# Optimization experiments

Measured on AMD Instinct MI355X. Metric: run time of the kernel, lower is better.

Reference implementation:

```python
import jax, jax.numpy as jnp
import numpy as np

P = 8  # patch size
EPS = 1e-5

def ln_ch(x, w, b):
    # WithBias LayerNorm over channel dim of (B,C,H,W): torch code flattens to (B,HW,C) and norms last dim
    mu = x.mean(axis=1, keepdims=True)
    var = ((x - mu) ** 2).mean(axis=1, keepdims=True)
    return (x - mu) / jnp.sqrt(var + EPS) * w[None, :, None, None] + b[None, :, None, None]

def conv1x1(x, w):
    # w: [C_out, C_in]
    return jnp.einsum('bchw,oc->bohw', x, w)

def dwconv3x3(x, w):
    # depthwise 3x3, w: [C,1,3,3]
    return jax.lax.conv_general_dilated(x, w, (1, 1), 'SAME', dimension_numbers=('NCHW', 'OIHW', 'NCHW'), feature_group_count=x.shape[1])

def patchify(x):
    b, c, H, W = x.shape
    return x.reshape(b, c, H // P, P, W // P, P).transpose(0, 1, 2, 4, 3, 5)  # b c h w p1 p2

def unpatchify(x):
    b, c, h, w, p1, p2 = x.shape
    return x.transpose(0, 1, 2, 4, 3, 5).reshape(b, c, h * p1, w * p2)

def setup_inputs() -> dict:
    key = jax.random.key(0)
    ks = jax.random.split(key, 16)
    B, C, H, W = 4, 64, 256, 256
    hid = 2 * C  # ffn_expansion_factor=2
    s = 0.02
    return {
        'x': jax.random.normal(ks[0], (B, C, H, W), jnp.float32),
        'evt': jax.random.normal(ks[1], (B, C, H, W), jnp.float32),
        'ln1i_w': jnp.ones((C,), jnp.float32), 'ln1i_b': jnp.zeros((C,), jnp.float32),
        'ln1e_w': jnp.ones((C,), jnp.float32), 'ln1e_b': jnp.zeros((C,), jnp.float32),
        'w_q': jax.random.normal(ks[2], (2 * C, C), jnp.float32) * s,
        'dw_q': jax.random.normal(ks[3], (2 * C, 1, 3, 3), jnp.float32) * s,
        'w_kv': jax.random.normal(ks[4], (4 * C, C), jnp.float32) * s,
        'dw_kv': jax.random.normal(ks[5], (4 * C, 1, 3, 3), jnp.float32) * s,
        'lnA_w': jnp.ones((2 * C,), jnp.float32), 'lnA_b': jnp.zeros((2 * C,), jnp.float32),
        'w_po_attn': jax.random.normal(ks[6], (C, 2 * C), jnp.float32) * s,
        'ln2_w': jnp.ones((C,), jnp.float32), 'ln2_b': jnp.zeros((C,), jnp.float32),
        'w_pi': jax.random.normal(ks[7], (2 * hid, C), jnp.float32) * s,
        'fft_param': jnp.ones((2 * hid, 1, 1, P, P // 2 + 1), jnp.float32),
        'dw_ffn': jax.random.normal(ks[8], (2 * hid, 1, 3, 3), jnp.float32) * s,
        'w_po_ffn': jax.random.normal(ks[9], (C, hid), jnp.float32) * s,
    }

def reference(x, evt, ln1i_w, ln1i_b, ln1e_w, ln1e_b, w_q, dw_q, w_kv, dw_kv, lnA_w, lnA_b, w_po_attn, ln2_w, ln2_b, w_pi, fft_param, dw_ffn, w_po_ffn):
    # ---- EventFSAS cross attention ----
    xn = ln_ch(x, ln1i_w, ln1i_b)
    en = ln_ch(evt, ln1e_w, ln1e_b)
    q = dwconv3x3(conv1x1(xn, w_q), dw_q)               # (B,2C,H,W)
    kv = dwconv3x3(conv1x1(en, w_kv), dw_kv)            # (B,4C,H,W)
    k, v = jnp.split(kv, 2, axis=1)
    qf = jnp.fft.rfft2(patchify(q))                      # (B,2C,h,w,8,5) complex
    kf = jnp.fft.rfft2(patchify(k))
    out = jnp.fft.irfft2(qf * kf, s=(P, P))
    out = ln_ch(unpatchify(out), lnA_w, lnA_b)
    x = x + conv1x1(v * out, w_po_attn)
    # ---- DFFN ----
    y = conv1x1(ln_ch(x, ln2_w, ln2_b), w_pi)            # (B,4C,H,W)
    yf = jnp.fft.rfft2(patchify(y)) * fft_param
    y = unpatchify(jnp.fft.irfft2(yf, s=(P, P)))
    y = dwconv3x3(y, dw_ffn)
    y1, y2 = jnp.split(y, 2, axis=1)
    y = jax.nn.gelu(y1, approximate=False) * y2          # torch nn.GELU is exact erf form
    return x + conv1x1(y, w_po_ffn)
```

## Files before the change

kernel.cpp:

```cpp
#include <hip/hip_runtime.h>

#define HW 65536
#define NPOS 262144

typedef unsigned int   u32;
typedef unsigned short u16;
typedef __attribute__((ext_vector_type(8))) short v8s;
typedef __attribute__((ext_vector_type(4))) float f32x4;
typedef __attribute__((ext_vector_type(2))) float f32x2;

__device__ __forceinline__ float bf2f(u16 h){
  union { u32 u; float f; } c; c.u = ((u32)h) << 16; return c.f;
}
__device__ __forceinline__ u16 f2bf(float f){
  union { u32 u; float f; } c; c.f = f;
  u32 r = c.u + 0x7fffu + ((c.u >> 16) & 1u);
  return (u16)(r >> 16);
}
__device__ __forceinline__ u32 pk2(float a, float b){
  return (u32)f2bf(a) | ((u32)f2bf(b) << 16);
}
__device__ __forceinline__ v8s as8(uint4 u){
  union { uint4 a; v8s b; } c; c.a = u; return c.b;
}
__device__ __forceinline__ f32x2 up2(u32 u){
  union { u32 u; float f; } lo, hi;
  lo.u = u << 16; hi.u = u & 0xffff0000u;
  f32x2 r; r.x = lo.f; r.y = hi.f; return r;
}
__device__ __forceinline__ float gelu_exact(float x){
  return 0.5f*x*(1.0f+erff(x*0.70710678118654752f));
}

__device__ void fold_w(const float* __restrict__ W, int rows,
                       const float* __restrict__ lw, const float* __restrict__ lb,
                       u16* __restrict__ Wf, float* __restrict__ A, float* __restrict__ B){
  int tid = threadIdx.x;
  for (int e = tid; e < rows*64; e += 256) Wf[e] = f2bf(lw[e & 63] * W[e]);
  for (int r = tid; r < rows; r += 256){
    float a = 0.f, b2 = 0.f;
    for (int c = 0; c < 64; c++){ float w = W[r*64+c]; a += lw[c]*w; b2 += lb[c]*w; }
    A[r] = a; B[r] = b2;
  }
}

__global__ void k_prep(const float* __restrict__ M, float* __restrict__ g,
    const float* wq,  const float* l1iw, const float* l1ib, u16* wqf,  float* aq,  float* bq,
    const float* wkv, const float* l1ew, const float* l1eb, u16* wkvf, float* akv, float* bkv,
    const float* wpi, const float* l2w,  const float* l2b,  u16* wpif, float* api, float* bpi,
    const float* wpa, u16* wpaf, const float* wpf, u16* wpff)
{
  int blk = blockIdx.x, tid = threadIdx.x;
  if (blk < 64){
    int t = blk*256 + tid;
    int c = t >> 6, uv = t & 63, u = uv >> 3, v = uv & 7;
    const float* mc = M + c*40;
    const float ctab[8] = {1.f, 0.70710678118654752f, 0.f, -0.70710678118654752f,
                           -1.f, -0.70710678118654752f, 0.f, 0.70710678118654752f};
    float acc = 0.f;
    for (int k1=0;k1<8;k1++)
      for (int k2=0;k2<8;k2++){
        float s = (k2<=4) ? mc[k1*5+k2] : mc[(((8-k1)&7)*5) + (8-k2)];
        acc += s * ctab[(k1*u + k2*v)&7];
      }
    g[t] = acc * (1.f/64.f);
  } else if (blk == 64){ fold_w(wq, 128, l1iw, l1ib, wqf, aq, bq); }
  else if (blk == 65){ fold_w(wkv, 256, l1ew, l1eb, wkvf, akv, bkv); }
  else if (blk == 66){ fold_w(wpi, 256, l2w, l2b, wpif, api, bpi); }
  else if (blk == 67){ for (int e=tid; e<64*128; e+=256) wpaf[e] = f2bf(wpa[e]); }
  else               { for (int e=tid; e<64*128; e+=256) wpff[e] = f2bf(wpf[e]); }
}

__global__ void k_prep2(const float* __restrict__ g, u16* __restrict__ CM){
  int c = blockIdx.x;
  const float* gc = g + (size_t)c*64;
  u16* cm = CM + (size_t)c*4096;
  for (int e = threadIdx.x; e < 4096; e += 256){
    int o = e >> 6, i = e & 63;
    int du = ((o>>3) - (i>>3)) & 7, dv = ((o&7) - (i&7)) & 7;
    cm[e] = f2bf(gc[du*8 + dv]);
  }
}

struct GA {
  const float* src; const u16* Wf; const float* Af; const float* Bf;
  u32* dst; int o0; int dstOffP; int Cdp; int b0; int pxbase;
};

template<int NZ>
__global__ __launch_bounds__(256) void k_gemm64(GA a0, GA a1){
  GA a = (blockIdx.y == 0) ? a0 : a1;
  __shared__ uint4 lsX[128*8];
  __shared__ uint4 lsW[64*NZ*8];
  __shared__ float2 sPart[256];
  __shared__ float2 sStat[128];
  int tid = threadIdx.x;
  int px = tid & 127, hf = tid >> 7;
  int p0 = a.pxbase + blockIdx.x*128;
  int b = p0 >> 16, hwb = p0 & 65535;
  {
    const uint4* wsrc = (const uint4*)(a.Wf + (size_t)a.o0*64);
    #pragma unroll
    for (int i=0; i<NZ*2; i++){
      int idx = i*256 + tid, row = idx>>3, s = idx&7;
      lsW[row*8 + (s ^ (row&7))] = wsrc[idx];
    }
  }
  {
    const float* sp = a.src + (size_t)b*64*HW + hwb + px + (size_t)(hf*32)*HW;
    float e[32];
    #pragma unroll
    for (int c=0;c<32;c++) e[c] = sp[(size_t)c*HW];
    float sm = 0.f, sq = 0.f;
    #pragma unroll
    for (int c=0;c<32;c++){ sm += e[c]; sq += e[c]*e[c]; }
    uint4* xrow = lsX + px*8;
    #pragma unroll
    for (int sl=0; sl<4; sl++){
      uint4 pkv;
      pkv.x = pk2(e[sl*8+0], e[sl*8+1]); pkv.y = pk2(e[sl*8+2], e[sl*8+3]);
      pkv.z = pk2(e[sl*8+4], e[sl*8+5]); pkv.w = pk2(e[sl*8+6], e[sl*8+7]);
      xrow[(hf*4+sl) ^ (px&7)] = pkv;
    }
    sPart[tid] = make_float2(sm, sq);
  }
  __syncthreads();
  if (tid < 128){
    float2 A = sPart[tid], B = sPart[tid+128];
    float s = A.x + B.x, q = A.y + B.y;
    float mu = s*(1.f/64.f);
    float var = q*(1.f/64.f) - mu*mu;
    sStat[tid] = make_float2(mu, rsqrtf(fmaxf(var,0.f)+1e-5f));
  }
  __syncthreads();
  int w = tid>>6, l = tid&63, g = l>>4, c15 = l&15;
  float2 stv[2];
  #pragma unroll
  for (int pp=0;pp<2;pp++) stv[pp] = sStat[w*32 + pp*16 + c15];

  #pragma unroll
  for (int z=0; z<NZ; z++){
    f32x4 acc[2][4];
    #pragma unroll
    for (int pp=0;pp<2;pp++)
      #pragma unroll
      for (int po=0;po<4;po++) acc[pp][po] = (f32x4){0.f,0.f,0.f,0.f};
    #pragma unroll
    for (int kk=0; kk<2; kk++){
      v8s wf[4], xf[2];
      #pragma unroll
      for (int po=0;po<4;po++){ int row = z*64 + po*16 + c15; wf[po] = as8(lsW[row*8 + ((kk*4+g) ^ (row&7))]); }
      #pragma unroll
      for (int pp=0;pp<2;pp++){ int row = w*32 + pp*16 + c15; xf[pp] = as8(lsX[row*8 + ((kk*4+g) ^ (row&7))]); }
      #pragma unroll
      for (int pp=0;pp<2;pp++)
        #pragma unroll
        for (int po=0;po<4;po++)
          acc[pp][po] = __builtin_amdgcn_mfma_f32_16x16x32_bf16(wf[po], xf[pp], acc[pp][po], 0,0,0);
    }
    size_t obaseP = ((size_t)(b - a.b0)*a.Cdp + a.dstOffP + z*32)*HW + hwb + w*32;
    #pragma unroll
    for (int po=0;po<4;po++)
      #pragma unroll
      for (int j2=0;j2<2;j2++){
        int oc = po*16 + g*4 + j2*2;
        float A0 = a.Af[a.o0 + z*64 + oc],   B0 = a.Bf[a.o0 + z*64 + oc];
        float A1 = a.Af[a.o0 + z*64 + oc+1], B1 = a.Bf[a.o0 + z*64 + oc+1];
        int ocp = po*8 + g*2 + j2;
        u32* dp = a.dst + obaseP + (size_t)ocp*HW + c15;
        #pragma unroll
        for (int pp=0;pp<2;pp++){
          float lo = stv[pp].y*(acc[pp][po][j2*2  ] - stv[pp].x*A0) + B0;
          float hi = stv[pp].y*(acc[pp][po][j2*2+1] - stv[pp].x*A1) + B1;
          dp[pp*16] = pk2(lo, hi);
        }
      }
  }
}

__global__ __launch_bounds__(256) void k_gemm_attn(
    const float* __restrict__ x, const u32* __restrict__ orawp, const u32* __restrict__ vbp,
    const float* __restrict__ lnw, const float* __restrict__ lnb,
    const u16* __restrict__ Wf, float* __restrict__ out)
{
  __shared__ uint4 lsX[128*16];
  __shared__ uint4 lsW[64*16];
  __shared__ float2 sPart[256];
  __shared__ float2 sStat[128];
  int tid = threadIdx.x;
  int p0 = blockIdx.x*128;
  int b = p0 >> 16, hwb = p0 & 65535;
  int px = tid & 127, hf = tid >> 7;
  {
    const uint4* wsrc = (const uint4*)Wf;
    #pragma unroll
    for (int i=0;i<4;i++){
      int idx = i*256 + tid, row = idx>>4, s = idx&15;
      lsW[row*16 + (s ^ (row&15))] = wsrc[idx];
    }
  }
  const u32* orp = orawp + ((size_t)b*64 + hf*32)*HW + hwb + px;
  {
    u32 r32[32];
    #pragma unroll
    for (int i=0;i<32;i++) r32[i] = orp[(size_t)i*HW];
    float sum = 0.f, ssq = 0.f;
    #pragma unroll
    for (int sl=0; sl<8; sl++){
      u32 wds[4];
      #pragma unroll
      for (int q2=0;q2<4;q2++){
        u32 wv = r32[sl*4+q2];
        float fl = bf2f((u16)(wv&0xffff)), fh = bf2f((u16)(wv>>16));
        sum += fl + fh; ssq += fl*fl + fh*fh;
        wds[q2] = wv;
      }
      int s = hf*8 + sl;
      lsX[px*16 + (s ^ (px&15))] = make_uint4(wds[0],wds[1],wds[2],wds[3]);
    }
    sPart[tid] = make_float2(sum, ssq);
  }
  __syncthreads();
  if (tid < 128){
    float2 A = sPart[tid], B = sPart[tid+128];
    float s = A.x + B.x, q = A.y + B.y;
    float mu = s*(1.f/128.f);
    float var = q*(1.f/128.f) - mu*mu;
    sStat[tid] = make_float2(mu, rsqrtf(fmaxf(var,0.f)+1e-5f));
  }
  __syncthreads();
  {
    float2 st = sStat[px];
    const u32* vp = vbp + ((size_t)b*64 + hf*32)*HW + hwb + px;
    u32 v32[32];
    #pragma unroll
    for (int i=0;i<32;i++) v32[i] = vp[(size_t)i*HW];
    #pragma unroll
    for (int sl=0; sl<8; sl++){
      int s = hf*8 + sl;
      int li = px*16 + (s ^ (px&15));
      uint4 raw = lsX[li];
      u32 wds[4] = {raw.x, raw.y, raw.z, raw.w};
      u32 ow[4];
      #pragma unroll
      for (int q2=0;q2<4;q2++){
        int ch = hf*64 + sl*8 + q2*2;
        float e0 = bf2f((u16)(wds[q2]&0xffff)), e1 = bf2f((u16)(wds[q2]>>16));
        u32 vv = v32[sl*4+q2];
        float v0 = bf2f((u16)(vv&0xffff)), v1 = bf2f((u16)(vv>>16));
        float r0 = ((e0-st.x)*st.y*lnw[ch  ] + lnb[ch  ])*v0;
        float r1 = ((e1-st.x)*st.y*lnw[ch+1] + lnb[ch+1])*v1;
        ow[q2] = pk2(r0, r1);
      }
      lsX[li] = make_uint4(ow[0],ow[1],ow[2],ow[3]);
    }
  }
  __syncthreads();
  int w4 = tid>>6, l = tid&63, g = l>>4, c15 = l&15;
  f32x4 acc[2][4];
  #pragma unroll
  for (int pp=0;pp<2;pp++)
    #pragma unroll
    for (int po=0;po<4;po++) acc[pp][po] = (f32x4){0.f,0.f,0.f,0.f};
  #pragma unroll
  for (int kk=0; kk<4; kk++){
    v8s wf[4], xf[2];
    #pragma unroll
    for (int po=0;po<4;po++){ int row = po*16 + c15; wf[po] = as8(lsW[row*16 + ((kk*4+g) ^ (row&15))]); }
    #pragma unroll
    for (int pp=0;pp<2;pp++){ int row = w4*32 + pp*16 + c15; xf[pp] = as8(lsX[row*16 + ((kk*4+g) ^ (row&15))]); }
    #pragma unroll
    for (int pp=0;pp<2;pp++)
      #pragma unroll
      for (int po=0;po<4;po++)
        acc[pp][po] = __builtin_amdgcn_mfma_f32_16x16x32_bf16(wf[po], xf[pp], acc[pp][po], 0,0,0);
  }
  size_t obase = (size_t)b*64*HW + hwb + w4*32;
  #pragma unroll
  for (int po=0;po<4;po++)
    #pragma unroll
    for (int j=0;j<4;j++){
      int oc = po*16 + g*4 + j;
      const float* xs = x + obase + (size_t)oc*HW + c15;
      float* dp = out + obase + (size_t)oc*HW + c15;
      #pragma unroll
      for (int pp=0;pp<2;pp++) dp[pp*16] = xs[pp*16] + acc[pp][po][j];
    }
}

__global__ __launch_bounds__(256) void k_gemm_ffn(
    const u32* __restrict__ y3gp, const u16* __restrict__ Wf, float* __restrict__ out,
    int pxbase, int b0)
{
  __shared__ uint4 lsX[128*16];
  __shared__ uint4 lsW[64*16];
  int tid = threadIdx.x;
  int p0 = pxbase + blockIdx.x*128;
  int b = p0 >> 16, hwb = p0 & 65535;
  int px = tid & 127, hf = tid >> 7;
  {
    const uint4* wsrc = (const uint4*)Wf;
    #pragma unroll
    for (int i=0;i<4;i++){
      int idx = i*256 + tid, row = idx>>4, s = idx&15;
      lsW[row*16 + (s ^ (row&15))] = wsrc[idx];
    }
  }
  const u32* yp = y3gp + ((size_t)(b-b0)*64 + hf*32)*HW + hwb + px;
  {
    u32 r32[32];
    #pragma unroll
    for (int i=0;i<32;i++) r32[i] = yp[(size_t)i*HW];
    #pragma unroll
    for (int sl=0; sl<8; sl++){
      int s = hf*8 + sl;
      lsX[px*16 + (s ^ (px&15))] = make_uint4(r32[sl*4+0],r32[sl*4+1],r32[sl*4+2],r32[sl*4+3]);
    }
  }
  __syncthreads();
  int w4 = tid>>6, l = tid&63, g = l>>4, c15 = l&15;
  f32x4 acc[2][4];
  #pragma unroll
  for (int pp=0;pp<2;pp++)
    #pragma unroll
    for (int po=0;po<4;po++) acc[pp][po] = (f32x4){0.f,0.f,0.f,0.f};
  #pragma unroll
  for (int kk=0; kk<4; kk++){
    v8s wf[4], xf[2];
    #pragma unroll
    for (int po=0;po<4;po++){ int row = po*16 + c15; wf[po] = as8(lsW[row*16 + ((kk*4+g) ^ (row&15))]); }
    #pragma unroll
    for (int pp=0;pp<2;pp++){ int row = w4*32 + pp*16 + c15; xf[pp] = as8(lsX[row*16 + ((kk*4+g) ^ (row&15))]); }
    #pragma unroll
    for (int pp=0;pp<2;pp++)
      #pragma unroll
      for (int po=0;po<4;po++)
        acc[pp][po] = __builtin_amdgcn_mfma_f32_16x16x32_bf16(wf[po], xf[pp], acc[pp][po], 0,0,0);
  }
  size_t obase = (size_t)b*64*HW + hwb + w4*32;
  #pragma unroll
  for (int po=0;po<4;po++)
    #pragma unroll
    for (int j=0;j<4;j++){
      int oc = po*16 + g*4 + j;
      float* dp = out + obase + (size_t)oc*HW + c15;
      #pragma unroll
      for (int pp=0;pp<2;pp++) dp[pp*16] = dp[pp*16] + acc[pp][po][j];
    }
}

__device__ __forceinline__ void dw8p_acc2(const u32* __restrict__ sp,
    const float* __restrict__ w9lo, const float* __restrict__ w9hi,
    int h, int w8, f32x2 a2[8])
{
  #pragma unroll
  for (int r=0;r<3;r++){
    int hh = h + r - 1;
    if (hh < 0 || hh > 255) continue;
    const u32* rp = sp + hh*256 + w8;
    uint4 ua = *(const uint4*)rp;
    uint4 ub = *(const uint4*)(rp+4);
    u32 e[8] = {ua.x,ua.y,ua.z,ua.w,ub.x,ub.y,ub.z,ub.w};
    u32 lef = (w8 > 0)   ? rp[-1] : 0u;
    u32 rig = (w8 < 248) ? rp[8]  : 0u;
    f32x2 vm[10];
    vm[0] = up2(lef);
    #pragma unroll
    for (int j=0;j<8;j++) vm[j+1] = up2(e[j]);
    vm[9] = up2(rig);
    f32x2 wa = {w9lo[r*3  ], w9hi[r*3  ]};
    f32x2 wb = {w9lo[r*3+1], w9hi[r*3+1]};
    f32x2 wc = {w9lo[r*3+2], w9hi[r*3+2]};
    #pragma unroll
    for (int j=0;j<8;j++)
      a2[j] += vm[j]*wa + vm[j+1]*wb + vm[j+2]*wc;
  }
}

__global__ __launch_bounds__(256) void k_dw8p(
    const u32* __restrict__ src, const float* __restrict__ wgt, int c0,
    u32* __restrict__ dstp, int dstOffP)
{
  int t = blockIdx.x*256 + threadIdx.x;
  int w8 = (t & 31)*8, h = (t>>5) & 255;
  int plane = t >> 13;
  int pr = plane & 31, b = plane >> 5;
  const u32* sp = src + (size_t)plane*HW;
  const float* w9 = wgt + (size_t)(c0 + 2*pr)*9;
  f32x2 a2[8];
  #pragma unroll
  for (int j=0;j<8;j++) a2[j] = (f32x2){0.f,0.f};
  dw8p_acc2(sp, w9, w9+9, h, w8, a2);
  u32* dp = dstp + ((size_t)(b*64 + dstOffP + pr))*HW + h*256 + w8;
  uint4 s0, s1;
  s0.x=pk2(a2[0].x,a2[0].y); s0.y=pk2(a2[1].x,a2[1].y); s0.z=pk2(a2[2].x,a2[2].y); s0.w=pk2(a2[3].x,a2[3].y);
  s1.x=pk2(a2[4].x,a2[4].y); s1.y=pk2(a2[5].x,a2[5].y); s1.z=pk2(a2[6].x,a2[6].y); s1.w=pk2(a2[7].x,a2[7].y);
  *(uint4*)dp = s0; *(uint4*)(dp+4) = s1;
}

__global__ __launch_bounds__(256) void k_dw8gp(
    const u32* __restrict__ Y0p, const float* __restrict__ wgt, u32* __restrict__ Y3gp)
{
  int t = blockIdx.x*256 + threadIdx.x;
  int w8 = (t & 31)*8, h = (t>>5) & 255;
  int pc = t >> 13;
  int pr = pc & 63, bl = pc >> 6;
  const u32* spA = Y0p + ((size_t)(bl*128 + pr))*HW;
  const u32* spG = Y0p + ((size_t)(bl*128 + 64 + pr))*HW;
  const float* w9a = wgt + (size_t)(2*pr)*9;
  const float* w9g = wgt + (size_t)(128 + 2*pr)*9;
  f32x2 aA[8], aG[8];
  #pragma unroll
  for (int j=0;j<8;j++){ aA[j] = (f32x2){0.f,0.f}; aG[j] = (f32x2){0.f,0.f}; }
  dw8p_acc2(spA, w9a, w9a+9, h, w8, aA);
  dw8p_acc2(spG, w9g, w9g+9, h, w8, aG);
  u32* dp = Y3gp + ((size_t)(bl*64 + pr))*HW + h*256 + w8;
  uint4 s0, s1;
  s0.x=pk2(gelu_exact(aA[0].x)*aG[0].x, gelu_exact(aA[0].y)*aG[0].y);
  s0.y=pk2(gelu_exact(aA[1].x)*aG[1].x, gelu_exact(aA[1].y)*aG[1].y);
  s0.z=pk2(gelu_exact(aA[2].x)*aG[2].x, gelu_exact(aA[2].y)*aG[2].y);
  s0.w=pk2(gelu_exact(aA[3].x)*aG[3].x, gelu_exact(aA[3].y)*aG[3].y);
  s1.x=pk2(gelu_exact(aA[4].x)*aG[4].x, gelu_exact(aA[4].y)*aG[4].y);
  s1.y=pk2(gelu_exact(aA[5].x)*aG[5].x, gelu_exact(aA[5].y)*aG[5].y);
  s1.z=pk2(gelu_exact(aA[6].x)*aG[6].x, gelu_exact(aA[6].y)*aG[6].y);
  s1.w=pk2(gelu_exact(aA[7].x)*aG[7].x, gelu_exact(aA[7].y)*aG[7].y);
  *(uint4*)dp = s0; *(uint4*)(dp+4) = s1;
}

__global__ __launch_bounds__(256) void k_circqk4(
    const u32* __restrict__ bq, const u32* __restrict__ bk,
    const float* __restrict__ dwq, const float* __restrict__ dwk, int c0,
    u32* __restrict__ orawp, int oprBase)
{
  __shared__ f32x2 qd[8][288];
  __shared__ f32x2 kd[8][288];
  int tid = threadIdx.x;
  int p = tid & 31, i = tid >> 5;
  int pr = blockIdx.y, b = blockIdx.z;
  int h0 = blockIdx.x*8;
  const u32* qp = bq + ((size_t)(b*32+pr))*HW;
  const u32* kp = bk + ((size_t)(b*32+pr))*HW;
  const float* wq9 = dwq + (size_t)(c0 + 2*pr)*9;
  const float* wk9 = dwk + (size_t)(c0 + 2*pr)*9;
  {
    f32x2 a2[8];
    #pragma unroll
    for (int j=0;j<8;j++) a2[j] = (f32x2){0.f,0.f};
    dw8p_acc2(qp, wq9, wq9+9, h0+i, p*8, a2);
    #pragma unroll
    for (int j=0;j<8;j++) qd[i][p*9+j] = a2[j];
  }
  {
    f32x2 a2[8];
    #pragma unroll
    for (int j=0;j<8;j++) a2[j] = (f32x2){0.f,0.f};
    dw8p_acc2(kp, wk9, wk9+9, h0+i, p*8, a2);
    #pragma unroll
    for (int j=0;j<8;j++) kd[i][p*9+j] = a2[j];
  }
  __syncthreads();
  f32x2 o[8];
  #pragma unroll
  for (int j=0;j<8;j++) o[j] = (f32x2){0.f,0.f};
  #pragma unroll
  for (int u=0;u<8;u++){
    int ku = (i-u)&7;
    f32x2 qv[8], kr[8];
    #pragma unroll
    for (int v=0;v<8;v++) qv[v] = qd[u][p*9+v];
    #pragma unroll
    for (int e=0;e<8;e++) kr[e] = kd[ku][p*9+e];
    #pragma unroll
    for (int v=0;v<8;v++){
      f32x2 qq = qv[v];
      #pragma unroll
      for (int j=0;j<8;j++)
        o[j] += qq * kr[(j-v)&7];
    }
  }
  u32* op = orawp + ((size_t)(b*64 + oprBase + pr))*HW + (size_t)(h0+i)*256 + p*8;
  uint4 s0, s1;
  s0.x=pk2(o[0].x,o[0].y); s0.y=pk2(o[1].x,o[1].y); s0.z=pk2(o[2].x,o[2].y); s0.w=pk2(o[3].x,o[3].y);
  s1.x=pk2(o[4].x,o[4].y); s1.y=pk2(o[5].x,o[5].y); s1.z=pk2(o[6].x,o[6].y); s1.w=pk2(o[7].x,o[7].y);
  *(uint4*)op = s0; *(uint4*)(op+4) = s1;
}

__global__ __launch_bounds__(256) void k_circg_mfma(
    u32* __restrict__ y, const u16* __restrict__ CM)
{
  __shared__ uint4 lsA[2][64*8];
  __shared__ uint4 lsB[2][64*8];
  int tid = threadIdx.x;
  int pr = blockIdx.y, b = blockIdx.z;
  int h0 = blockIdx.x*16;
  u32* plane = y + ((size_t)(b*128+pr))*HW;
  {
    const uint4* cmsrc = (const uint4*)(CM + (size_t)(2*pr)*4096);
    #pragma unroll
    for (int t=0; t<4; t++){
      int idx = t*256 + tid;
      int ch = idx >> 9, e = idx & 511;
      int row = e >> 3, s = e & 7;
      lsA[ch][row*8 + (s ^ (row&7))] = cmsrc[ch*512 + e];
    }
  }
  {
    #pragma unroll
    for (int t=0; t<2; t++){
      int rr = t*256 + tid;
      int n = rr >> 3, i = rr & 7;
      const u32* rp = plane + (size_t)(h0 + (n>>5)*8 + i)*256 + (n&31)*8;
      uint4 ua = *(const uint4*)rp;
      uint4 ub = *(const uint4*)(rp+4);
      u32 e[8] = {ua.x,ua.y,ua.z,ua.w,ub.x,ub.y,ub.z,ub.w};
      uint4 L, H;
      L.x = (e[0]&0xffffu) | (e[1]<<16);
      L.y = (e[2]&0xffffu) | (e[3]<<16);
      L.z = (e[4]&0xffffu) | (e[5]<<16);
      L.w = (e[6]&0xffffu) | (e[7]<<16);
      H.x = (e[0]>>16) | (e[1]&0xffff0000u);
      H.y = (e[2]>>16) | (e[3]&0xffff0000u);
      H.z = (e[4]>>16) | (e[5]&0xffff0000u);
      H.w = (e[6]>>16) | (e[7]&0xffff0000u);
      lsB[0][n*8 + (i ^ (n&7))] = L;
      lsB[1][n*8 + (i ^ (n&7))] = H;
    }
  }
  __syncthreads();
  int w = tid>>6, l = tid&63, g = l>>4, c15 = l&15;
  f32x4 acc[2][4];
  #pragma unroll
  for (int ch=0;ch<2;ch++)
    #pragma unroll
    for (int po=0;po<4;po++) acc[ch][po] = (f32x4){0.f,0.f,0.f,0.f};
  #pragma unroll
  for (int kk=0; kk<2; kk++){
    v8s bfr[2];
    { int row = w*16 + c15;
      bfr[0] = as8(lsB[0][row*8 + ((kk*4+g) ^ (row&7))]);
      bfr[1] = as8(lsB[1][row*8 + ((kk*4+g) ^ (row&7))]); }
    #pragma unroll
    for (int po=0;po<4;po++){
      int row = po*16 + c15;
      v8s aL = as8(lsA[0][row*8 + ((kk*4+g) ^ (row&7))]);
      v8s aH = as8(lsA[1][row*8 + ((kk*4+g) ^ (row&7))]);
      acc[0][po] = __builtin_amdgcn_mfma_f32_16x16x32_bf16(aL, bfr[0], acc[0][po], 0,0,0);
      acc[1][po] = __builtin_amdgcn_mfma_f32_16x16x32_bf16(aH, bfr[1], acc[1][po], 0,0,0);
    }
  }
  int patch = w*16 + c15;
  u32* pbase = plane + (size_t)(h0 + (patch>>5)*8)*256 + (patch&31)*8;
  #pragma unroll
  for (int po=0;po<4;po++){
    int oh = po*2 + (g>>1), ow4 = 4*(g&1);
    uint4 sv;
    sv.x = pk2(acc[0][po][0], acc[1][po][0]);
    sv.y = pk2(acc[0][po][1], acc[1][po][1]);
    sv.z = pk2(acc[0][po][2], acc[1][po][2]);
    sv.w = pk2(acc[0][po][3], acc[1][po][3]);
    *(uint4*)(pbase + (size_t)oh*256 + ow4) = sv;
  }
}

extern "C" void kernel_launch(void* const* d_in, const int* in_sizes, int n_in,
                              void* d_out, int out_size, void* d_ws, size_t ws_size,
                              hipStream_t stream)
{
  const float* x       = (const float*)d_in[0];
  const float* evt     = (const float*)d_in[1];
  const float* ln1i_w  = (const float*)d_in[2];
  const float* ln1i_b  = (const float*)d_in[3];
  const float* ln1e_w  = (const float*)d_in[4];
  const float* ln1e_b  = (const float*)d_in[5];
  const float* w_q     = (const float*)d_in[6];
  const float* dw_q    = (const float*)d_in[7];
  const float* w_kv    = (const float*)d_in[8];
  const float* dw_kv   = (const float*)d_in[9];
  const float* lnA_w   = (const float*)d_in[10];
  const float* lnA_b   = (const float*)d_in[11];
  const float* w_po_at = (const float*)d_in[12];
  const float* ln2_w   = (const float*)d_in[13];
  const float* ln2_b   = (const float*)d_in[14];
  const float* w_pi    = (const float*)d_in[15];
  const float* fft_par = (const float*)d_in[16];
  const float* dw_ffn  = (const float*)d_in[17];
  const float* w_poffn = (const float*)d_in[18];
  float* out = (float*)d_out;

  char* ws = (char*)d_ws;
  const size_t MiB = 1048576ull;
  u32*   P1p   = (u32*)(ws);
  u32*   ORAWp = (u32*)(ws + 32*MiB);
  u32*   P2p   = (u32*)(ws + 96*MiB);
  u32*   VBUFp = (u32*)(ws + 96*MiB);
  u32*   Y0p   = (u32*)(ws);
  u32*   Y3Gp  = (u32*)(ws + 64*MiB);
  char* sm = ws + 160*MiB;
  float* G    = (float*)(sm);
  u16* WQF    = (u16*)(sm + 65536);
  u16* WKVF   = (u16*)(sm + 81920);
  u16* WPIF   = (u16*)(sm + 114688);
  u16* WPAF   = (u16*)(sm + 147456);
  u16* WPFF   = (u16*)(sm + 163840);
  float* AQ   = (float*)(sm + 180224);
  float* BQ   = (float*)(sm + 180736);
  float* AKV  = (float*)(sm + 181248);
  float* BKV  = (float*)(sm + 182272);
  float* API  = (float*)(sm + 183296);
  float* BPI  = (float*)(sm + 184320);
  u16* CMAT   = (u16*)(ws + 161*MiB);

  dim3 blk256(256);

  k_prep<<<69, blk256, 0, stream>>>(fft_par, G,
      w_q, ln1i_w, ln1i_b, WQF, AQ, BQ,
      w_kv, ln1e_w, ln1e_b, WKVF, AKV, BKV,
      w_pi, ln2_w, ln2_b, WPIF, API, BPI,
      w_po_at, WPAF, w_poffn, WPFF);
  k_prep2<<<256, blk256, 0, stream>>>(G, CMAT);

  for (int i=0;i<2;i++){
    GA qa = {x,   WQF,  AQ,  BQ,  P1p, 64*i, 0, 32, 0, 0};
    GA ka = {evt, WKVF, AKV, BKV, P2p, 64*i, 0, 32, 0, 0};
    k_gemm64<1><<<dim3(2048,2,1), blk256, 0, stream>>>(qa, ka);
    k_circqk4<<<dim3(32,32,4), blk256, 0, stream>>>(P1p, P2p, dw_q, dw_kv, 64*i, ORAWp, 32*i);
  }
  for (int i=0;i<2;i++){
    GA va = {evt, WKVF, AKV, BKV, P1p, 128+64*i, 0, 32, 0, 0};
    k_gemm64<1><<<dim3(2048,1,1), blk256, 0, stream>>>(va, va);
    k_dw8p<<<4096, blk256, 0, stream>>>(P1p, dw_kv, 128+64*i, VBUFp, 32*i);
  }
  k_gemm_attn<<<2048, blk256, 0, stream>>>(x, ORAWp, VBUFp, lnA_w, lnA_b, WPAF, out);

  for (int h=0;h<2;h++){
    GA pa = {out, WPIF, API, BPI, Y0p, 0, 0, 128, 2*h, h*131072};
    k_gemm64<4><<<dim3(1024,1,1), blk256, 0, stream>>>(pa, pa);
    k_circg_mfma<<<dim3(16,128,2), blk256, 0, stream>>>(Y0p, CMAT);
    k_dw8gp<<<4096, blk256, 0, stream>>>(Y0p, dw_ffn, Y3Gp);
    k_gemm_ffn<<<1024, blk256, 0, stream>>>(Y3Gp, WPFF, out, h*131072, 2*h);
  }
}
```

Baseline: 523.5 us.

## Process all Q/K/V channel chunks in one pass when workspace allows

When the workspace holds at least 200 MiB, the attention stage computes all 64 channel pairs per GEMM and circular-conv launch. This replaces the two half-width chunks, so it uses fewer launches and re-reads the x/evt inputs and layernorm stats fewer times. The workspace layout is remapped so the larger Q, K and ORAW buffers fit, and constant tables move to a higher offset. The old chunked path is kept as a fallback for smaller workspaces. Whether the new path runs depends on the workspace size the harness provides.

```diff
diff --git a/kernel.cpp b/kernel.cpp
--- a/kernel.cpp
+++ b/kernel.cpp
@@ -379,12 +379,12 @@
 
 __global__ __launch_bounds__(256) void k_dw8p(
     const u32* __restrict__ src, const float* __restrict__ wgt, int c0,
-    u32* __restrict__ dstp, int dstOffP)
+    u32* __restrict__ dstp, int dstOffP, int prMask, int prShift)
 {
   int t = blockIdx.x*256 + threadIdx.x;
   int w8 = (t & 31)*8, h = (t>>5) & 255;
   int plane = t >> 13;
-  int pr = plane & 31, b = plane >> 5;
+  int pr = plane & prMask, b = plane >> prShift;
   const u32* sp = src + (size_t)plane*HW;
   const float* w9 = wgt + (size_t)(c0 + 2*pr)*9;
   f32x2 a2[8];
@@ -430,7 +430,7 @@
 __global__ __launch_bounds__(256) void k_circqk4(
     const u32* __restrict__ bq, const u32* __restrict__ bk,
     const float* __restrict__ dwq, const float* __restrict__ dwk, int c0,
-    u32* __restrict__ orawp, int oprBase)
+    u32* __restrict__ orawp, int oprBase, int cpb)
 {
   __shared__ f32x2 qd[8][288];
   __shared__ f32x2 kd[8][288];
@@ -438,8 +438,8 @@
   int p = tid & 31, i = tid >> 5;
   int pr = blockIdx.y, b = blockIdx.z;
   int h0 = blockIdx.x*8;
-  const u32* qp = bq + ((size_t)(b*32+pr))*HW;
-  const u32* kp = bk + ((size_t)(b*32+pr))*HW;
+  const u32* qp = bq + ((size_t)(b*cpb+pr))*HW;
+  const u32* kp = bk + ((size_t)(b*cpb+pr))*HW;
   const float* wq9 = dwq + (size_t)(c0 + 2*pr)*9;
   const float* wk9 = dwk + (size_t)(c0 + 2*pr)*9;
   {
@@ -589,13 +589,9 @@
 
   char* ws = (char*)d_ws;
   const size_t MiB = 1048576ull;
-  u32*   P1p   = (u32*)(ws);
-  u32*   ORAWp = (u32*)(ws + 32*MiB);
-  u32*   P2p   = (u32*)(ws + 96*MiB);
-  u32*   VBUFp = (u32*)(ws + 96*MiB);
-  u32*   Y0p   = (u32*)(ws);
-  u32*   Y3Gp  = (u32*)(ws + 64*MiB);
-  char* sm = ws + 160*MiB;
+  bool big = (ws_size >= 200*MiB);
+  size_t smOff = big ? 192*MiB : 160*MiB;
+  char* sm = ws + smOff;
   float* G    = (float*)(sm);
   u16* WQF    = (u16*)(sm + 65536);
   u16* WKVF   = (u16*)(sm + 81920);
@@ -608,7 +604,7 @@
   float* BKV  = (float*)(sm + 182272);
   float* API  = (float*)(sm + 183296);
   float* BPI  = (float*)(sm + 184320);
-  u16* CMAT   = (u16*)(ws + 161*MiB);
+  u16* CMAT   = (u16*)(sm + 1*MiB);
 
   dim3 blk256(256);
 
@@ -619,24 +615,56 @@
       w_po_at, WPAF, w_poffn, WPFF);
   k_prep2<<<256, blk256, 0, stream>>>(G, CMAT);
 
-  for (int i=0;i<2;i++){
-    GA qa = {x,   WQF,  AQ,  BQ,  P1p, 64*i, 0, 32, 0, 0};
-    GA ka = {evt, WKVF, AKV, BKV, P2p, 64*i, 0, 32, 0, 0};
-    k_gemm64<1><<<dim3(2048,2,1), blk256, 0, stream>>>(qa, ka);
-    k_circqk4<<<dim3(32,32,4), blk256, 0, stream>>>(P1p, P2p, dw_q, dw_kv, 64*i, ORAWp, 32*i);
-  }
-  for (int i=0;i<2;i++){
-    GA va = {evt, WKVF, AKV, BKV, P1p, 128+64*i, 0, 32, 0, 0};
-    k_gemm64<1><<<dim3(2048,1,1), blk256, 0, stream>>>(va, va);
-    k_dw8p<<<4096, blk256, 0, stream>>>(P1p, dw_kv, 128+64*i, VBUFp, 32*i);
-  }
-  k_gemm_attn<<<2048, blk256, 0, stream>>>(x, ORAWp, VBUFp, lnA_w, lnA_b, WPAF, out);
-
-  for (int h=0;h<2;h++){
-    GA pa = {out, WPIF, API, BPI, Y0p, 0, 0, 128, 2*h, h*131072};
-    k_gemm64<4><<<dim3(1024,1,1), blk256, 0, stream>>>(pa, pa);
-    k_circg_mfma<<<dim3(16,128,2), blk256, 0, stream>>>(Y0p, CMAT);
-    k_dw8gp<<<4096, blk256, 0, stream>>>(Y0p, dw_ffn, Y3Gp);
-    k_gemm_ffn<<<1024, blk256, 0, stream>>>(Y3Gp, WPFF, out, h*131072, 2*h);
-  }
-}
+  if (big){
+    u32* QBUF  = (u32*)(ws);
+    u32* KBUF  = (u32*)(ws + 64*MiB);
+    u32* ORAWp = (u32*)(ws + 128*MiB);
+    u32* PV    = (u32*)(ws + 64*MiB);
+    u32* VBUFp = (u32*)(ws);
+    u32* Y0p   = (u32*)(ws + 64*MiB);
+    u32* Y3Gp  = (u32*)(ws + 128*MiB);
+
+    GA qa = {x,   WQF,  AQ,  BQ,  QBUF, 0, 0, 64, 0, 0};
+    GA ka = {evt, WKVF, AKV, BKV, KBUF, 0, 0, 64, 0, 0};
+    k_gemm64<2><<<dim3(2048,2,1), blk256, 0, stream>>>(qa, ka);
+    k_circqk4<<<dim3(32,64,4), blk256, 0, stream>>>(QBUF, KBUF, dw_q, dw_kv, 0, ORAWp, 0, 64);
+    GA va = {evt, WKVF, AKV, BKV, PV, 128, 0, 64, 0, 0};
+    k_gemm64<2><<<dim3(2048,1,1), blk256, 0, stream>>>(va, va);
+    k_dw8p<<<8192, blk256, 0, stream>>>(PV, dw_kv, 128, VBUFp, 0, 63, 6);
+    k_gemm_attn<<<2048, blk256, 0, stream>>>(x, ORAWp, VBUFp, lnA_w, lnA_b, WPAF, out);
+    for (int h=0;h<2;h++){
+      GA pa = {out, WPIF, API, BPI, Y0p, 0, 0, 128, 2*h, h*131072};
+      k_gemm64<4><<<dim3(1024,1,1), blk256, 0, stream>>>(pa, pa);
+      k_circg_mfma<<<dim3(16,128,2), blk256, 0, stream>>>(Y0p, CMAT);
+      k_dw8gp<<<4096, blk256, 0, stream>>>(Y0p, dw_ffn, Y3Gp);
+      k_gemm_ffn<<<1024, blk256, 0, stream>>>(Y3Gp, WPFF, out, h*131072, 2*h);
+    }
+  } else {
+    u32* P1p   = (u32*)(ws);
+    u32* ORAWp = (u32*)(ws + 32*MiB);
+    u32* P2p   = (u32*)(ws + 96*MiB);
+    u32* VBUFp = (u32*)(ws + 96*MiB);
+    u32* Y0p   = (u32*)(ws);
+    u32* Y3Gp  = (u32*)(ws + 64*MiB);
+
+    for (int i=0;i<2;i++){
+      GA qa = {x,   WQF,  AQ,  BQ,  P1p, 64*i, 0, 32, 0, 0};
+      GA ka = {evt, WKVF, AKV, BKV, P2p, 64*i, 0, 32, 0, 0};
+      k_gemm64<1><<<dim3(2048,2,1), blk256, 0, stream>>>(qa, ka);
+      k_circqk4<<<dim3(32,32,4), blk256, 0, stream>>>(P1p, P2p, dw_q, dw_kv, 64*i, ORAWp, 32*i, 32);
+    }
+    for (int i=0;i<2;i++){
+      GA va = {evt, WKVF, AKV, BKV, P1p, 128+64*i, 0, 32, 0, 0};
+      k_gemm64<1><<<dim3(2048,1,1), blk256, 0, stream>>>(va, va);
+      k_dw8p<<<4096, blk256, 0, stream>>>(P1p, dw_kv, 128+64*i, VBUFp, 32*i, 31, 5);
+    }
+    k_gemm_attn<<<2048, blk256, 0, stream>>>(x, ORAWp, VBUFp, lnA_w, lnA_b, WPAF, out);
+    for (int h=0;h<2;h++){
+      GA pa = {out, WPIF, API, BPI, Y0p, 0, 0, 128, 2*h, h*131072};
+      k_gemm64<4><<<dim3(1024,1,1), blk256, 0, stream>>>(pa, pa);
+      k_circg_mfma<<<dim3(16,128,2), blk256, 0, stream>>>(Y0p, CMAT);
+      k_dw8gp<<<4096, blk256, 0, stream>>>(Y0p, dw_ffn, Y3Gp);
+      k_gemm_ffn<<<1024, blk256, 0, stream>>>(Y3Gp, WPFF, out, h*131072, 2*h);
+    }
+  }
+}
```

After: 477.8 us (median of 2 runs). 8.7% less time.
